# Kernel tuning notes

Hardware: AMD Instinct MI355X
Metric: run time of the kernel (lower is better)

Reference implementation:

```python
import jax, jax.numpy as jnp
import numpy as np

N_HEADS, INPUT_DIM, EMBED_DIM = 8, 128, 128
KEY_DIM = EMBED_DIM // N_HEADS  # val_dim = key_dim = 16
B, N = 8, 1024


def setup_inputs() -> dict:
    key = jax.random.key(0)
    ks = jax.random.split(key, 16)
    stdv_k = 1.0 / np.sqrt(KEY_DIM)
    stdv_e = 1.0 / np.sqrt(EMBED_DIM)

    def U(k, shape, s):
        return jax.random.uniform(k, shape, jnp.float32, -s, s)

    hdk = (N_HEADS, INPUT_DIM, KEY_DIM)
    hke = (N_HEADS, KEY_DIM, EMBED_DIM)
    return {
        "q_n": jax.random.normal(ks[0], (B, N, INPUT_DIM), jnp.float32),
        "q_c": jax.random.normal(ks[1], (B, N, INPUT_DIM), jnp.float32),
        "mask": jax.random.bernoulli(ks[2], 0.5, (B, N, N)),
        "W_query_n": U(ks[3], hdk, stdv_k),
        "W_key_nn": U(ks[4], hdk, stdv_k),
        "W_val_nn": U(ks[5], hdk, stdv_k),
        "W_key_c": U(ks[6], hdk, stdv_k),
        "W_val_c": U(ks[7], hdk, stdv_k),
        "W_query_c": U(ks[8], hdk, stdv_k),
        "W_key_n": U(ks[9], hdk, stdv_k),
        "W_val_n": U(ks[10], hdk, stdv_k),
        "W_out_node": U(ks[11], hke, stdv_e),
        "W_out_color": U(ks[12], hke, stdv_e),
    }


def reference(q_n, q_c, mask, W_query_n, W_key_nn, W_val_nn, W_key_c, W_val_c,
              W_query_c, W_key_n, W_val_n, W_out_node, W_out_color):
    norm = 1.0 / jnp.sqrt(jnp.asarray(KEY_DIM, q_n.dtype))
    neg_inf = jnp.asarray(-jnp.inf, q_n.dtype)

    def proj(x, W):  # (B,N,D), (H,D,K) -> (H,B,N,K)
        return jnp.einsum('bnd,hdk->hbnk', x, W)

    # --- color stream: q_c attends over nodes q_n ---
    Q_c = proj(q_c, W_query_c)
    K_n = proj(q_n, W_key_n)
    V_n = proj(q_n, W_val_n)
    attn_c = jax.nn.softmax(norm * jnp.einsum('hbqk,hbnk->hbqn', Q_c, K_n), axis=-1)
    heads_c = jnp.einsum('hbqn,hbnv->hbqv', attn_c, V_n)
    out_color = jnp.einsum('hbqv,hve->bqe', heads_c, W_out_color)

    # --- node stream: masked self-attention + attention over colors ---
    Q_n = proj(q_n, W_query_n)
    K_nn = proj(q_n, W_key_nn)
    V_nn = proj(q_n, W_val_nn)
    comp_nn = norm * jnp.einsum('hbqk,hbnk->hbqn', Q_n, K_nn)
    m = mask[None]  # (1,B,Q,N) broadcast over heads; True = not allowed
    comp_nn = jnp.where(m, neg_inf, comp_nn)
    attn_nn = jax.nn.softmax(comp_nn, axis=-1)
    attn_nn = jnp.where(m, jnp.asarray(0.0, q_n.dtype), attn_nn)
    heads_nn = jnp.einsum('hbqn,hbnv->hbqv', attn_nn, V_nn)

    K_nc = proj(q_c, W_key_c)
    V_nc = proj(q_c, W_val_c)
    attn_nc = jax.nn.softmax(norm * jnp.einsum('hbqk,hbnk->hbqn', Q_n, K_nc), axis=-1)
    heads_nc = jnp.einsum('hbqn,hbnv->hbqv', attn_nc, V_nc)

    heads = heads_nn + heads_nc
    out = jnp.einsum('hbqv,hve->bqe', heads, W_out_node)
    return (out, out_color)
```

## Files before the change

### kernel.cpp

```cpp
#include <hip/hip_runtime.h>
#include <stdint.h>

#define NH 8
#define NB 8
#define NN 1024
#define ND 128
#define NK 16
#define NF (NB*NN)
#define C2EXP 0.36067376022224085f
#define LSTR 136

typedef float f32x16 __attribute__((ext_vector_type(16)));
typedef short bf16x8 __attribute__((ext_vector_type(8)));

__device__ __forceinline__ uint16_t f2bf(float f){
  uint32_t x = __float_as_uint(f);
  uint32_t r = (x + 0x7fffu + ((x>>16)&1u)) >> 16;
  return (uint16_t)r;
}
__device__ __forceinline__ float fast_exp2(float x){
#if __has_builtin(__builtin_amdgcn_exp2f)
  return __builtin_amdgcn_exp2f(x);
#else
  return exp2f(x);
#endif
}

__global__ __launch_bounds__(256) void pack_kernel(const int* __restrict__ mask,
                                                   uint32_t* __restrict__ packN,
                                                   uint16_t* __restrict__ onesw){
  if (blockIdx.x == 0) {
    for (int i = threadIdx.x; i < 1024; i += 256) onesw[i] = 0x3F80;
  }
  const int w = threadIdx.x >> 6, lane = threadIdx.x & 63;
  const int row = blockIdx.x*4 + w;
  const int* mp = mask + (size_t)row*NN;
  uint32_t* dst = packN + (size_t)row*32;
  for (int wq = 0; wq < 16; ++wq) {
    int v = mp[wq*64 + lane];
    unsigned long long bal = __ballot(v != 0);
    if (lane == 0) { dst[wq*2] = (uint32_t)bal; dst[wq*2+1] = (uint32_t)(bal>>32); }
  }
}

struct ProjArgs { const float* x[8]; const float* w[8]; };

__global__ __launch_bounds__(256) void proj_kernel(ProjArgs args, uint16_t* ws){
  __shared__ __align__(16) uint16_t WT[128*LSTR];
  __shared__ __align__(16) uint16_t S[128*LSTR];
  const int p = blockIdx.y;
  const int rb = blockIdx.x;
  const int tid = threadIdx.x;

  const float4* w4 = (const float4*)args.w[p];
  #pragma unroll
  for (int i = 0; i < 16; ++i) {
    int e4 = i*256 + tid;
    float4 f = w4[e4];
    int e = e4*4;
    int h = e >> 11, d = (e >> 4) & 127, k = e & 15;
    uint16_t* wr = &WT[(h*16 + k)*LSTR + d];
    wr[0*LSTR] = f2bf(f.x); wr[1*LSTR] = f2bf(f.y);
    wr[2*LSTR] = f2bf(f.z); wr[3*LSTR] = f2bf(f.w);
  }
  __syncthreads();

  const int wave = tid >> 6, lane = tid & 63;
  const int l5 = lane >> 5, lm = lane & 31;
  const int r0 = rb*128 + wave*32;
  const float* xrow = args.x[p] + (size_t)(r0 + lm)*ND + l5*8;

  bf16x8 afr[8];
  #pragma unroll
  for (int kt = 0; kt < 8; ++kt) {
    float4 f0 = *(const float4*)(xrow + kt*16);
    float4 f1 = *(const float4*)(xrow + kt*16 + 4);
    bf16x8 a;
    a[0]=f2bf(f0.x); a[1]=f2bf(f0.y); a[2]=f2bf(f0.z); a[3]=f2bf(f0.w);
    a[4]=f2bf(f1.x); a[5]=f2bf(f1.y); a[6]=f2bf(f1.z); a[7]=f2bf(f1.w);
    afr[kt] = a;
  }

  const bool tr = (p==2)|(p==5)|(p==7);
  const float qsc = (p==0 || p==3) ? C2EXP : 1.0f;
  #pragma unroll
  for (int nt = 0; nt < 4; ++nt) {
    f32x16 acc;
    #pragma unroll
    for (int i = 0; i < 16; ++i) acc[i] = 0.f;
    #pragma unroll
    for (int kt = 0; kt < 8; ++kt) {
      bf16x8 b = *(const bf16x8*)(&WT[(nt*32 + lm)*LSTR + kt*16 + l5*8]);
      acc = __builtin_amdgcn_mfma_f32_32x32x16_bf16(afr[kt], b, acc, 0, 0, 0);
    }
    #pragma unroll
    for (int i = 0; i < 16; ++i) {
      int r = wave*32 + (i&3) + 8*(i>>2) + 4*l5;
      int c = nt*32 + lm;
      if (tr) {
        int t2 = (r>>2)&3;
        int rp = (t2==1 || t2==2) ? (r^12) : r;
        S[c*LSTR + rp] = f2bf(acc[i]);
      } else {
        S[r*LSTR + c] = f2bf(acc[i]*qsc);
      }
    }
  }
  __syncthreads();

  uint16_t* dst = ws + (size_t)p*((size_t)NH*NF*NK);
  if (!tr) {
    #pragma unroll
    for (int it = 0; it < 8; ++it) {
      int c = it*256 + tid;
      int row = c >> 4, cg = c & 15;
      bf16x8 v = *(const bf16x8*)(&S[row*LSTR + cg*8]);
      int h = cg >> 1, k8 = cg & 1;
      *(bf16x8*)(dst + ((size_t)h*NF + rb*128 + row)*NK + k8*8) = v;
    }
  } else {
    const int b = rb >> 3, nb = (rb & 7)*128;
    #pragma unroll
    for (int it = 0; it < 8; ++it) {
      int c = it*256 + tid;
      int col = c >> 4, ng = c & 15;
      bf16x8 v = *(const bf16x8*)(&S[col*LSTR + ng*8]);
      int h = col >> 4, k = col & 15;
      *(bf16x8*)(dst + ((size_t)(h*NB + b)*NK + k)*NN + nb + ng*8) = v;
    }
  }
}

template<bool MASKED>
__device__ __forceinline__ void attn_stream(
    const uint4* __restrict__ kbuf, bf16x8 aq,
    const uint16_t* __restrict__ vbase, const uint4* __restrict__ pmw4,
    int nh, int l5, int lm, f32x16& O)
{
  f32x16 Z;
  #pragma unroll
  for (int i = 0; i < 16; ++i) Z[i] = 0.f;

  uint32_t mw[16];
  if (MASKED) {
    uint4 m0 = pmw4[nh*4+0], m1 = pmw4[nh*4+1];
    uint4 m2 = pmw4[nh*4+2], m3 = pmw4[nh*4+3];
    mw[0]=m0.x; mw[1]=m0.y; mw[2]=m0.z; mw[3]=m0.w;
    mw[4]=m1.x; mw[5]=m1.y; mw[6]=m1.z; mw[7]=m1.w;
    mw[8]=m2.x; mw[9]=m2.y; mw[10]=m2.z; mw[11]=m2.w;
    mw[12]=m3.x; mw[13]=m3.y; mw[14]=m3.z; mw[15]=m3.w;
  }

  const int base_n = nh*512;
  const bool vload = (lm < 17);

  bf16x8 av1, av2, av1n, av2n;
  #pragma unroll
  for (int i = 0; i < 8; ++i) { av1[i]=0; av2[i]=0; av1n[i]=0; av2n[i]=0; }
  if (vload) {
    const uint16_t* vp = vbase + base_n + l5*8;
    av1 = *(const bf16x8*)(vp);
    av2 = *(const bf16x8*)(vp + 16);
  }
  f32x16 Stc = __builtin_amdgcn_mfma_f32_32x32x16_bf16(
      *(const bf16x8*)(&kbuf[l5*1024 + base_n + lm]), aq, Z, 0, 0, 0);

  #pragma unroll
  for (int t = 0; t < 16; ++t) {
    f32x16 Stn;
    if (t < 15) {
      const int n1 = base_n + (t+1)*32;
      if (vload) {
        const uint16_t* vp = vbase + n1 + l5*8;
        av1n = *(const bf16x8*)(vp);
        av2n = *(const bf16x8*)(vp + 16);
      }
      Stn = __builtin_amdgcn_mfma_f32_32x32x16_bf16(
          *(const bf16x8*)(&kbuf[l5*1024 + n1 + lm]), aq, Z, 0, 0, 0);
    }

    const uint32_t mws = MASKED ? (mw[t] >> (4*l5)) : 0u;
    float p[16];
    #pragma unroll
    for (int i = 0; i < 16; ++i) {
      float pv = fast_exp2(Stc[i]);
      if (MASKED && ((mws >> ((i&3) + 8*(i>>2))) & 1u)) pv = 0.f;
      p[i] = pv;
    }
    union { uint32_t u[4]; bf16x8 v; } B1, B2;
    #pragma unroll
    for (int k = 0; k < 4; ++k) {
      B1.u[k] = __builtin_amdgcn_perm(__float_as_uint(p[2*k+1]),
                                      __float_as_uint(p[2*k]),   0x07060302u);
      B2.u[k] = __builtin_amdgcn_perm(__float_as_uint(p[2*k+9]),
                                      __float_as_uint(p[2*k+8]), 0x07060302u);
    }
    O = __builtin_amdgcn_mfma_f32_32x32x16_bf16(av1, B1.v, O, 0, 0, 0);
    O = __builtin_amdgcn_mfma_f32_32x32x16_bf16(av2, B2.v, O, 0, 0, 0);

    if (t < 15) { Stc = Stn; av1 = av1n; av2 = av2n; }
  }
}

__global__ __launch_bounds__(512, 4) void attn_kernel(
    const uint16_t* __restrict__ Qn_, const uint16_t* __restrict__ K1n,
    const uint16_t* __restrict__ V1n, const uint16_t* __restrict__ K2n,
    const uint16_t* __restrict__ V2n,
    const uint16_t* __restrict__ Qc_, const uint16_t* __restrict__ K1c,
    const uint16_t* __restrict__ V1c,
    const uint32_t* __restrict__ packN, const uint16_t* __restrict__ onesb,
    uint16_t* __restrict__ hn_, uint16_t* __restrict__ hc_)
{
  __shared__ uint4 kbuf[2048];
  const bool dual = (blockIdx.z == 0);
  const uint16_t* Q   = dual ? Qn_ : Qc_;
  const uint16_t* K1  = dual ? K1n : K1c;
  uint16_t* outp      = dual ? hn_ : hc_;

  const int hb = blockIdx.y;
  const int h = hb >> 3, b = hb & 7;
  const size_t base = ((size_t)h*NF + (size_t)b*NN)*NK;
  const int tid = threadIdx.x;

  const uint4* k1 = (const uint4*)(K1 + base);
  for (int i = tid; i < 2048; i += 512)
    kbuf[(i & 1)*1024 + (i >> 1)] = k1[i];
  __syncthreads();

  const int wave = tid >> 6, lane = tid & 63;
  const int l5 = lane >> 5, lm = lane & 31;
  const int qt = wave & 3, nh = wave >> 2;
  const int q = blockIdx.x*128 + qt*32 + lm;

  const bf16x8 aq = *(const bf16x8*)(Q + base + (size_t)q*NK + l5*8);
  const uint4* pmw4 = (const uint4*)(packN + ((size_t)b*NN + q)*32);

  const uint16_t* VT1 = (dual ? V1n : V1c) + (size_t)hb*(NK*NN);
  const uint16_t* vb1 = (lm < 16) ? (VT1 + (size_t)lm*NN) : onesb;

  f32x16 O1, O2;
  #pragma unroll
  for (int i = 0; i < 16; ++i) { O1[i] = 0.f; O2[i] = 0.f; }

  if (dual) {
    attn_stream<true>(kbuf, aq, vb1, pmw4, nh, l5, lm, O1);
    __syncthreads();
    const uint4* k2 = (const uint4*)(K2n + base);
    for (int i = tid; i < 2048; i += 512)
      kbuf[(i & 1)*1024 + (i >> 1)] = k2[i];
    __syncthreads();
    const uint16_t* VT2 = V2n + (size_t)hb*(NK*NN);
    const uint16_t* vb2 = (lm < 16) ? (VT2 + (size_t)lm*NN) : onesb;
    attn_stream<false>(kbuf, aq, vb2, nullptr, nh, l5, lm, O2);
  } else {
    attn_stream<false>(kbuf, aq, vb1, nullptr, nh, l5, lm, O1);
  }

  float L1 = O1[8] + __shfl_xor(O1[8], 32, 64);
  float L2 = O2[8] + __shfl_xor(O2[8], 32, 64);

  __syncthreads();
  float* cw = ((float*)kbuf) + ((size_t)(qt*2 + l5)*32 + lm)*18;
  if (nh == 1) {
    #pragma unroll
    for (int i = 0; i < 8; ++i) cw[i] = O1[i];
    if (dual) {
      #pragma unroll
      for (int i = 0; i < 8; ++i) cw[8+i] = O2[i];
    }
    cw[16] = L1; cw[17] = L2;
  }
  __syncthreads();
  if (nh == 0) {
    const float l1 = L1 + cw[16];
    const float i1 = (l1 > 0.f) ? 1.f/l1 : 0.f;
    float i2 = 0.f;
    if (dual) { const float l2 = L2 + cw[17]; i2 = (l2 > 0.f) ? 1.f/l2 : 0.f; }
    uint32_t w[4];
    #pragma unroll
    for (int k = 0; k < 4; ++k) {
      float va = (O1[2*k]   + cw[2*k])  *i1;
      float vb = (O1[2*k+1] + cw[2*k+1])*i1;
      if (dual) { va += (O2[2*k] + cw[8+2*k])*i2; vb += (O2[2*k+1] + cw[8+2*k+1])*i2; }
      w[k] = ((uint32_t)f2bf(vb) << 16) | f2bf(va);
    }
    uint16_t* hp = outp + ((size_t)b*NN + q)*128 + h*16 + l5*4;
    *(uint2*)(hp)     = make_uint2(w[0], w[1]);
    *(uint2*)(hp + 8) = make_uint2(w[2], w[3]);
  }
}

__global__ __launch_bounds__(256) void outproj_kernel(
    const uint16_t* __restrict__ hn, const uint16_t* __restrict__ hc,
    const float* __restrict__ wn, const float* __restrict__ wc,
    float* __restrict__ out)
{
  __shared__ __align__(16) uint16_t WT[128*LSTR];
  const int s = blockIdx.y;
  const int rb = blockIdx.x;
  const int tid = threadIdx.x;
  const float* wsrc = s ? wc : wn;
  const float4* w4 = (const float4*)wsrc;
  #pragma unroll
  for (int i = 0; i < 16; ++i) {
    int e4 = i*256 + tid;
    float4 f = w4[e4];
    int e = e4*4;
    int c = e >> 7, col = e & 127;
    uint16_t* wr = &WT[col*LSTR + c];
    wr[0*LSTR] = f2bf(f.x); wr[1*LSTR] = f2bf(f.y);
    wr[2*LSTR] = f2bf(f.z); wr[3*LSTR] = f2bf(f.w);
  }
  __syncthreads();

  const int wave = tid >> 6, lane = tid & 63;
  const int l5 = lane >> 5, lm = lane & 31;
  const int rt = wave & 1, nh2 = wave >> 1;
  const int r0 = rb*64 + rt*32;
  const uint16_t* hp = (s ? hc : hn) + (size_t)(r0 + lm)*128 + l5*8;
  bf16x8 afr[8];
  #pragma unroll
  for (int kt = 0; kt < 8; ++kt) afr[kt] = *(const bf16x8*)(hp + kt*16);

  float* dst = out + (size_t)s*((size_t)NF*ND) + (size_t)r0*ND;
  #pragma unroll
  for (int nt2 = 0; nt2 < 2; ++nt2) {
    const int nt = nh2*2 + nt2;
    f32x16 acc;
    #pragma unroll
    for (int i = 0; i < 16; ++i) acc[i] = 0.f;
    #pragma unroll
    for (int kt = 0; kt < 8; ++kt) {
      bf16x8 b = *(const bf16x8*)(&WT[(nt*32 + lm)*LSTR + kt*16 + l5*8]);
      acc = __builtin_amdgcn_mfma_f32_32x32x16_bf16(afr[kt], b, acc, 0, 0, 0);
    }
    #pragma unroll
    for (int i = 0; i < 16; ++i) {
      int r = (i&3) + 8*(i>>2) + 4*l5;
      dst[(size_t)r*ND + nt*32 + lm] = acc[i];
    }
  }
}

extern "C" void kernel_launch(void* const* d_in, const int* in_sizes, int n_in,
                              void* d_out, int out_size, void* d_ws, size_t ws_size,
                              hipStream_t stream)
{
  const float* q_n = (const float*)d_in[0];
  const float* q_c = (const float*)d_in[1];
  const int* mask = (const int*)d_in[2];
  const float* W[10];
  for (int i = 0; i < 10; ++i) W[i] = (const float*)d_in[3+i];

  uint16_t* ws16 = (uint16_t*)d_ws;
  const size_t PE = (size_t)NH*NF*NK;
  uint16_t* Qc   = ws16 + 0*PE;
  uint16_t* Kn   = ws16 + 1*PE;
  uint16_t* VTn  = ws16 + 2*PE;
  uint16_t* Qn   = ws16 + 3*PE;
  uint16_t* Knn  = ws16 + 4*PE;
  uint16_t* VTnn = ws16 + 5*PE;
  uint16_t* Knc  = ws16 + 6*PE;
  uint16_t* VTnc = ws16 + 7*PE;
  uint16_t* heads_node = ws16 + 8*PE;
  uint32_t* packN   = (uint32_t*)(ws16 + 9*PE);
  uint16_t* heads_c = ws16 + 10*PE;
  uint16_t* onesb   = ws16 + 11*PE;

  pack_kernel<<<2048, 256, 0, stream>>>(mask, packN, onesb);

  ProjArgs pa;
  pa.x[0]=q_c; pa.w[0]=W[5];
  pa.x[1]=q_n; pa.w[1]=W[6];
  pa.x[2]=q_n; pa.w[2]=W[7];
  pa.x[3]=q_n; pa.w[3]=W[0];
  pa.x[4]=q_n; pa.w[4]=W[1];
  pa.x[5]=q_n; pa.w[5]=W[2];
  pa.x[6]=q_c; pa.w[6]=W[3];
  pa.x[7]=q_c; pa.w[7]=W[4];
  proj_kernel<<<dim3(64, 8), 256, 0, stream>>>(pa, ws16);

  attn_kernel<<<dim3(8, 64, 2), 512, 0, stream>>>(
      Qn, Knn, VTnn, Knc, VTnc, Qc, Kn, VTn, packN, onesb,
      heads_node, heads_c);

  outproj_kernel<<<dim3(128, 2), 256, 0, stream>>>(heads_node, heads_c,
                                                   W[8], W[9], (float*)d_out);
}
```

Before: 168.5 us.

## Split dual-stream attention blocks into separate balanced blocks and fuse sum in outproj

The node stream's two attention passes (masked self-attention and attention over colors) now run in separate blocks instead of sequentially in one block, giving three uniform work streams. Blocks shrink from 512 to 256 threads and cover 64 queries each. The heads_nn + heads_nc sum is deferred to the output projection, which issues a second MFMA per k-step into the same accumulator. This removes the load imbalance between dual and single blocks, at the cost of an extra bf16 heads buffer, extra K loads into LDS per block, and rounding each partial to bf16 before the sum.

```diff
diff --git a/kernel.cpp b/kernel.cpp
--- a/kernel.cpp
+++ b/kernel.cpp
@@ -202,87 +202,70 @@
   }
 }
 
-__global__ __launch_bounds__(512, 4) void attn_kernel(
-    const uint16_t* __restrict__ Qn_, const uint16_t* __restrict__ K1n,
-    const uint16_t* __restrict__ V1n, const uint16_t* __restrict__ K2n,
-    const uint16_t* __restrict__ V2n,
-    const uint16_t* __restrict__ Qc_, const uint16_t* __restrict__ K1c,
-    const uint16_t* __restrict__ V1c,
+__global__ __launch_bounds__(256, 4) void attn_kernel(
+    const uint16_t* __restrict__ Qn_, const uint16_t* __restrict__ Knn,
+    const uint16_t* __restrict__ VTnn, const uint16_t* __restrict__ Knc,
+    const uint16_t* __restrict__ VTnc,
+    const uint16_t* __restrict__ Qc_, const uint16_t* __restrict__ Kn,
+    const uint16_t* __restrict__ VTn,
     const uint32_t* __restrict__ packN, const uint16_t* __restrict__ onesb,
-    uint16_t* __restrict__ hn_, uint16_t* __restrict__ hc_)
+    uint16_t* __restrict__ hnn_, uint16_t* __restrict__ hnc_,
+    uint16_t* __restrict__ hc_)
 {
   __shared__ uint4 kbuf[2048];
-  const bool dual = (blockIdx.z == 0);
-  const uint16_t* Q   = dual ? Qn_ : Qc_;
-  const uint16_t* K1  = dual ? K1n : K1c;
-  uint16_t* outp      = dual ? hn_ : hc_;
-
-  const int hb = blockIdx.y;
-  const int h = hb >> 3, b = hb & 7;
+  const int z = blockIdx.z;
+  const uint16_t* Q  = (z == 2) ? Qc_ : Qn_;
+  const uint16_t* K  = (z == 0) ? Knn : (z == 1) ? Knc : Kn;
+  const uint16_t* VT = (z == 0) ? VTnn : (z == 1) ? VTnc : VTn;
+  uint16_t* outp     = (z == 0) ? hnn_ : (z == 1) ? hnc_ : hc_;
+
+  const int h = blockIdx.x >> 3, b = blockIdx.x & 7;
+  const int hb = h*8 + b;
   const size_t base = ((size_t)h*NF + (size_t)b*NN)*NK;
   const int tid = threadIdx.x;
 
-  const uint4* k1 = (const uint4*)(K1 + base);
-  for (int i = tid; i < 2048; i += 512)
+  const uint4* k1 = (const uint4*)(K + base);
+  for (int i = tid; i < 2048; i += 256)
     kbuf[(i & 1)*1024 + (i >> 1)] = k1[i];
   __syncthreads();
 
   const int wave = tid >> 6, lane = tid & 63;
   const int l5 = lane >> 5, lm = lane & 31;
-  const int qt = wave & 3, nh = wave >> 2;
-  const int q = blockIdx.x*128 + qt*32 + lm;
+  const int qt = wave & 1, nh = wave >> 1;
+  const int q = blockIdx.y*64 + qt*32 + lm;
 
   const bf16x8 aq = *(const bf16x8*)(Q + base + (size_t)q*NK + l5*8);
   const uint4* pmw4 = (const uint4*)(packN + ((size_t)b*NN + q)*32);
 
-  const uint16_t* VT1 = (dual ? V1n : V1c) + (size_t)hb*(NK*NN);
-  const uint16_t* vb1 = (lm < 16) ? (VT1 + (size_t)lm*NN) : onesb;
-
-  f32x16 O1, O2;
-  #pragma unroll
-  for (int i = 0; i < 16; ++i) { O1[i] = 0.f; O2[i] = 0.f; }
-
-  if (dual) {
-    attn_stream<true>(kbuf, aq, vb1, pmw4, nh, l5, lm, O1);
-    __syncthreads();
-    const uint4* k2 = (const uint4*)(K2n + base);
-    for (int i = tid; i < 2048; i += 512)
-      kbuf[(i & 1)*1024 + (i >> 1)] = k2[i];
-    __syncthreads();
-    const uint16_t* VT2 = V2n + (size_t)hb*(NK*NN);
-    const uint16_t* vb2 = (lm < 16) ? (VT2 + (size_t)lm*NN) : onesb;
-    attn_stream<false>(kbuf, aq, vb2, nullptr, nh, l5, lm, O2);
-  } else {
-    attn_stream<false>(kbuf, aq, vb1, nullptr, nh, l5, lm, O1);
-  }
-
-  float L1 = O1[8] + __shfl_xor(O1[8], 32, 64);
-  float L2 = O2[8] + __shfl_xor(O2[8], 32, 64);
-
-  __syncthreads();
-  float* cw = ((float*)kbuf) + ((size_t)(qt*2 + l5)*32 + lm)*18;
+  const uint16_t* VTb = VT + (size_t)hb*(NK*NN);
+  const uint16_t* vb = (lm < 16) ? (VTb + (size_t)lm*NN) : onesb;
+
+  f32x16 O;
+  #pragma unroll
+  for (int i = 0; i < 16; ++i) O[i] = 0.f;
+
+  if (z == 0) attn_stream<true >(kbuf, aq, vb, pmw4,   nh, l5, lm, O);
+  else        attn_stream<false>(kbuf, aq, vb, nullptr, nh, l5, lm, O);
+
+  float L1 = O[8] + __shfl_xor(O[8], 32, 64);
+
+  __syncthreads();
+  float* cw = ((float*)kbuf) + (size_t)((qt*2 + l5)*32 + lm)*9;
   if (nh == 1) {
     #pragma unroll
-    for (int i = 0; i < 8; ++i) cw[i] = O1[i];
-    if (dual) {
-      #pragma unroll
-      for (int i = 0; i < 8; ++i) cw[8+i] = O2[i];
-    }
-    cw[16] = L1; cw[17] = L2;
+    for (int i = 0; i < 8; ++i) cw[i] = O[i];
+    cw[8] = L1;
   }
   __syncthreads();
   if (nh == 0) {
-    const float l1 = L1 + cw[16];
+    const float l1 = L1 + cw[8];
     const float i1 = (l1 > 0.f) ? 1.f/l1 : 0.f;
-    float i2 = 0.f;
-    if (dual) { const float l2 = L2 + cw[17]; i2 = (l2 > 0.f) ? 1.f/l2 : 0.f; }
     uint32_t w[4];
     #pragma unroll
     for (int k = 0; k < 4; ++k) {
-      float va = (O1[2*k]   + cw[2*k])  *i1;
-      float vb = (O1[2*k+1] + cw[2*k+1])*i1;
-      if (dual) { va += (O2[2*k] + cw[8+2*k])*i2; vb += (O2[2*k+1] + cw[8+2*k+1])*i2; }
-      w[k] = ((uint32_t)f2bf(vb) << 16) | f2bf(va);
+      float va = (O[2*k]   + cw[2*k])  *i1;
+      float vb2 = (O[2*k+1] + cw[2*k+1])*i1;
+      w[k] = ((uint32_t)f2bf(vb2) << 16) | f2bf(va);
     }
     uint16_t* hp = outp + ((size_t)b*NN + q)*128 + h*16 + l5*4;
     *(uint2*)(hp)     = make_uint2(w[0], w[1]);
@@ -291,7 +274,8 @@
 }
 
 __global__ __launch_bounds__(256) void outproj_kernel(
-    const uint16_t* __restrict__ hn, const uint16_t* __restrict__ hc,
+    const uint16_t* __restrict__ hnn, const uint16_t* __restrict__ hnc,
+    const uint16_t* __restrict__ hc,
     const float* __restrict__ wn, const float* __restrict__ wc,
     float* __restrict__ out)
 {
@@ -317,10 +301,16 @@
   const int l5 = lane >> 5, lm = lane & 31;
   const int rt = wave & 1, nh2 = wave >> 1;
   const int r0 = rb*64 + rt*32;
-  const uint16_t* hp = (s ? hc : hn) + (size_t)(r0 + lm)*128 + l5*8;
-  bf16x8 afr[8];
-  #pragma unroll
-  for (int kt = 0; kt < 8; ++kt) afr[kt] = *(const bf16x8*)(hp + kt*16);
+  const size_t hoff = (size_t)(r0 + lm)*128 + l5*8;
+  const uint16_t* hp1 = (s ? hc : hnn) + hoff;
+  bf16x8 afr[8], afr2[8];
+  #pragma unroll
+  for (int kt = 0; kt < 8; ++kt) afr[kt] = *(const bf16x8*)(hp1 + kt*16);
+  if (!s) {
+    const uint16_t* hp2 = hnc + hoff;
+    #pragma unroll
+    for (int kt = 0; kt < 8; ++kt) afr2[kt] = *(const bf16x8*)(hp2 + kt*16);
+  }
 
   float* dst = out + (size_t)s*((size_t)NF*ND) + (size_t)r0*ND;
   #pragma unroll
@@ -333,6 +323,7 @@
     for (int kt = 0; kt < 8; ++kt) {
       bf16x8 b = *(const bf16x8*)(&WT[(nt*32 + lm)*LSTR + kt*16 + l5*8]);
       acc = __builtin_amdgcn_mfma_f32_32x32x16_bf16(afr[kt], b, acc, 0, 0, 0);
+      if (!s) acc = __builtin_amdgcn_mfma_f32_32x32x16_bf16(afr2[kt], b, acc, 0, 0, 0);
     }
     #pragma unroll
     for (int i = 0; i < 16; ++i) {
@@ -362,10 +353,11 @@
   uint16_t* VTnn = ws16 + 5*PE;
   uint16_t* Knc  = ws16 + 6*PE;
   uint16_t* VTnc = ws16 + 7*PE;
-  uint16_t* heads_node = ws16 + 8*PE;
+  uint16_t* hnn  = ws16 + 8*PE;
   uint32_t* packN   = (uint32_t*)(ws16 + 9*PE);
-  uint16_t* heads_c = ws16 + 10*PE;
-  uint16_t* onesb   = ws16 + 11*PE;
+  uint16_t* onesb   = ws16 + 9*PE + 524288;
+  uint16_t* hc   = ws16 + 10*PE;
+  uint16_t* hnc  = ws16 + 11*PE;
 
   pack_kernel<<<2048, 256, 0, stream>>>(mask, packN, onesb);
 
@@ -380,10 +372,10 @@
   pa.x[7]=q_c; pa.w[7]=W[4];
   proj_kernel<<<dim3(64, 8), 256, 0, stream>>>(pa, ws16);
 
-  attn_kernel<<<dim3(8, 64, 2), 512, 0, stream>>>(
+  attn_kernel<<<dim3(64, 16, 3), 256, 0, stream>>>(
       Qn, Knn, VTnn, Knc, VTnc, Qc, Kn, VTn, packN, onesb,
-      heads_node, heads_c);
-
-  outproj_kernel<<<dim3(128, 2), 256, 0, stream>>>(heads_node, heads_c,
+      hnn, hnc, hc);
+
+  outproj_kernel<<<dim3(128, 2), 256, 0, stream>>>(hnn, hnc, hc,
                                                    W[8], W[9], (float*)d_out);
 }
```

Measured after the change: 165.4 us. No clear change (-1.8%).
